# Performance work log

Hardware: AMD Instinct MI355X
Metric: run time of the kernel (lower is better)

The kernel has to match this reference:

```python
import jax, jax.numpy as jnp
import numpy as np

N, D, H, E = 16384, 2048, 1024, 16  # tokens, d_model, hidden_size, num_experts


def setup_inputs() -> dict:
    key = jax.random.key(0)
    k1, k2, k3 = jax.random.split(key, 3)
    x = jax.random.normal(k1, (N, D), dtype=jnp.float32)
    w_up_gate = jax.random.normal(k2, (E, 2 * H, D), dtype=jnp.float32) * 0.02
    w_down = jax.random.normal(k3, (E, H, D), dtype=jnp.float32) * 0.02
    # Tokens are pre-sorted by expert; uniform routing: N // E tokens per expert.
    batch_size_per_expert = jnp.full((E,), N // E, dtype=jnp.int32)
    return {
        "x": x,
        "w_up_gate": w_up_gate,
        "w_down": w_down,
        "batch_size_per_expert": batch_size_per_expert,
    }


def reference(x, w_up_gate, w_down, batch_size_per_expert):
    # Grouped GEMM expert FFN with SwiGLU (high-precision math path of
    # RoutedExperts.forward). Groups are uniform (N // E tokens each), so the
    # grouped matmul gmm(x, w.T, batch_sizes) is exactly a batched einsum over
    # the expert-contiguous token blocks.
    n_experts = w_up_gate.shape[0]
    hidden = w_down.shape[1]
    xg = x.reshape(n_experts, -1, x.shape[-1])            # [E, T, D]
    # up-gate projection: x_e @ w_up_gate[e].T -> [E, T, 2H]
    up_gate = jnp.einsum("etd,ehd->eth", xg, w_up_gate)
    up = up_gate[..., :hidden]                             # [E, T, H]
    gate = up_gate[..., hidden:]                           # [E, T, H]
    h = up * jax.nn.silu(gate)                             # fused SwiGLU
    # down projection: h_e @ w_down[e] -> [E, T, D]
    down = jnp.einsum("eth,ehd->etd", h, w_down)
    return down.reshape(x.shape)
```

## Files before the change

kernel.cpp:

```cpp
#include <hip/hip_runtime.h>
#include <hip/hip_bf16.h>

#define NE 16
#define NT 1024
#define ND 2048
#define NH 1024

typedef __bf16 bf16x8 __attribute__((ext_vector_type(8)));
typedef __bf16 bf16x4 __attribute__((ext_vector_type(4)));
typedef float  f32x4  __attribute__((ext_vector_type(4)));

__device__ __forceinline__ void async_load16(const __bf16* g, __bf16* l) {
  __builtin_amdgcn_global_load_lds(
      (const __attribute__((address_space(1))) void*)g,
      (__attribute__((address_space(3))) void*)l, 16, 0, 0);
}

template<bool CBF16>
__global__ __launch_bounds__(256, 2)
void gemm_nt_lds(const __bf16* __restrict__ Ap, const __bf16* __restrict__ Bp,
                 void* __restrict__ Cp, int K, long sA, long sB, long sC)
{
  __shared__ __bf16 As[128 * 32];
  __shared__ __bf16 Bs[128 * 32];

  const int tid  = threadIdx.x;
  const int lane = tid & 63;
  const int wave = tid >> 6;
  const int wr = wave >> 1, wc = wave & 1;
  const int m0 = blockIdx.y * 128;
  const int n0 = blockIdx.x * 128;
  const long zb = blockIdx.z;

  const __bf16* A = Ap + zb * sA + (long)m0 * K;
  const __bf16* B = Bp + zb * sB + (long)n0 * K;

  const int sr = lane >> 2;
  const int sc = (lane & 3) * 8;

  f32x4 acc[4][4] = {};
  const int kq  = (lane >> 4) * 8;
  const int l15 = lane & 15;

  for (int kk = 0; kk < K; kk += 32) {
    #pragma unroll
    for (int p = 0; p < 2; ++p) {
      const int slab = wave * 2 + p;
      const int r = slab * 16 + sr;
      async_load16(A + (long)r * K + kk + sc, &As[slab * 512]);
      async_load16(B + (long)r * K + kk + sc, &Bs[slab * 512]);
    }
    __syncthreads();

    bf16x8 af[4], bq[4];
    #pragma unroll
    for (int i = 0; i < 4; ++i)
      af[i] = *(const bf16x8*)(&As[(wr * 64 + i * 16 + l15) * 32 + kq]);
    #pragma unroll
    for (int j = 0; j < 4; ++j)
      bq[j] = *(const bf16x8*)(&Bs[(wc * 64 + j * 16 + l15) * 32 + kq]);
    #pragma unroll
    for (int i = 0; i < 4; ++i)
      #pragma unroll
      for (int j = 0; j < 4; ++j)
        acc[i][j] = __builtin_amdgcn_mfma_f32_16x16x32_bf16(af[i], bq[j], acc[i][j], 0, 0, 0);
    __syncthreads();
  }

  const int rq = (lane >> 4) * 4;
  if constexpr (CBF16) {
    __bf16* C = (__bf16*)Cp + zb * sC;
    #pragma unroll
    for (int i = 0; i < 4; ++i)
      #pragma unroll
      for (int j = 0; j < 4; ++j)
        #pragma unroll
        for (int r = 0; r < 4; ++r)
          C[(long)(m0 + wr * 64 + i * 16 + rq + r) * 2048 +
            (n0 + wc * 64 + j * 16 + l15)] = (__bf16)acc[i][j][r];
  } else {
    float* C = (float*)Cp + zb * sC;
    #pragma unroll
    for (int i = 0; i < 4; ++i)
      #pragma unroll
      for (int j = 0; j < 4; ++j)
        #pragma unroll
        for (int r = 0; r < 4; ++r)
          C[(long)(m0 + wr * 64 + i * 16 + rq + r) * 2048 +
            (n0 + wc * 64 + j * 16 + l15)] = acc[i][j][r];
  }
}

constexpr int LDSS = 40;
template<bool AF32, bool BF32, bool CBF16>
__global__ __launch_bounds__(256, 2)
void gemm_nt(const void* __restrict__ Ap, const void* __restrict__ Bp,
             void* __restrict__ Cp, int K, long sA, long sB, long sC)
{
  __shared__ __bf16 As[128 * LDSS];
  __shared__ __bf16 Bs[128 * LDSS];
  const int tid  = threadIdx.x;
  const int lane = tid & 63;
  const int wave = tid >> 6;
  const int wr = wave >> 1, wc = wave & 1;
  const int m0 = blockIdx.y * 128;
  const int n0 = blockIdx.x * 128;
  const long zb = blockIdx.z;
  f32x4 acc[4][4] = {};
  const int kq  = (lane >> 4) * 8;
  const int l15 = lane & 15;

  for (int kk = 0; kk < K; kk += 32) {
    if constexpr (AF32) {
      const float* A = (const float*)Ap + zb * sA + (long)m0 * K + kk;
      #pragma unroll
      for (int p = 0; p < 4; ++p) {
        const int r = p * 32 + (tid >> 3);
        const int c = (tid & 7) * 4;
        const float4 v = *(const float4*)(A + (long)r * K + c);
        bf16x4 w;
        w[0] = (__bf16)v.x; w[1] = (__bf16)v.y; w[2] = (__bf16)v.z; w[3] = (__bf16)v.w;
        *(bf16x4*)(&As[r * LDSS + c]) = w;
      }
    } else {
      const __bf16* A = (const __bf16*)Ap + zb * sA + (long)m0 * K + kk;
      #pragma unroll
      for (int p = 0; p < 2; ++p) {
        const int r = p * 64 + (tid >> 2);
        const int c = (tid & 3) * 8;
        *(bf16x8*)(&As[r * LDSS + c]) = *(const bf16x8*)(A + (long)r * K + c);
      }
    }
    if constexpr (BF32) {
      const float* B = (const float*)Bp + zb * sB + (long)n0 * K + kk;
      #pragma unroll
      for (int p = 0; p < 4; ++p) {
        const int r = p * 32 + (tid >> 3);
        const int c = (tid & 7) * 4;
        const float4 v = *(const float4*)(B + (long)r * K + c);
        bf16x4 w;
        w[0] = (__bf16)v.x; w[1] = (__bf16)v.y; w[2] = (__bf16)v.z; w[3] = (__bf16)v.w;
        *(bf16x4*)(&Bs[r * LDSS + c]) = w;
      }
    } else {
      const __bf16* B = (const __bf16*)Bp + zb * sB + (long)n0 * K + kk;
      #pragma unroll
      for (int p = 0; p < 2; ++p) {
        const int r = p * 64 + (tid >> 2);
        const int c = (tid & 3) * 8;
        *(bf16x8*)(&Bs[r * LDSS + c]) = *(const bf16x8*)(B + (long)r * K + c);
      }
    }
    __syncthreads();
    bf16x8 af[4], bq[4];
    #pragma unroll
    for (int i = 0; i < 4; ++i)
      af[i] = *(const bf16x8*)(&As[(wr * 64 + i * 16 + l15) * LDSS + kq]);
    #pragma unroll
    for (int j = 0; j < 4; ++j)
      bq[j] = *(const bf16x8*)(&Bs[(wc * 64 + j * 16 + l15) * LDSS + kq]);
    #pragma unroll
    for (int i = 0; i < 4; ++i)
      #pragma unroll
      for (int j = 0; j < 4; ++j)
        acc[i][j] = __builtin_amdgcn_mfma_f32_16x16x32_bf16(af[i], bq[j], acc[i][j], 0, 0, 0);
    __syncthreads();
  }
  const int rq = (lane >> 4) * 4;
  if constexpr (CBF16) {
    __bf16* C = (__bf16*)Cp + zb * sC;
    #pragma unroll
    for (int i = 0; i < 4; ++i)
      #pragma unroll
      for (int j = 0; j < 4; ++j)
        #pragma unroll
        for (int r = 0; r < 4; ++r)
          C[(long)(m0 + wr * 64 + i * 16 + rq + r) * 2048 +
            (n0 + wc * 64 + j * 16 + l15)] = (__bf16)acc[i][j][r];
  } else {
    float* C = (float*)Cp + zb * sC;
    #pragma unroll
    for (int i = 0; i < 4; ++i)
      #pragma unroll
      for (int j = 0; j < 4; ++j)
        #pragma unroll
        for (int r = 0; r < 4; ++r)
          C[(long)(m0 + wr * 64 + i * 16 + rq + r) * 2048 +
            (n0 + wc * 64 + j * 16 + l15)] = acc[i][j][r];
  }
}

__global__ __launch_bounds__(256)
void cast_f32_bf16(const float* __restrict__ src, __bf16* __restrict__ dst)
{
  const long i = ((long)blockIdx.x * 256 + threadIdx.x) * 8;
  const float4 a = *(const float4*)(src + i);
  const float4 b = *(const float4*)(src + i + 4);
  bf16x8 o;
  o[0] = (__bf16)a.x; o[1] = (__bf16)a.y; o[2] = (__bf16)a.z; o[3] = (__bf16)a.w;
  o[4] = (__bf16)b.x; o[5] = (__bf16)b.y; o[6] = (__bf16)b.z; o[7] = (__bf16)b.w;
  *(bf16x8*)(dst + i) = o;
}

__global__ __launch_bounds__(256)
void transpose_cast_wdown(const float* __restrict__ w, __bf16* __restrict__ wt)
{
  __shared__ __bf16 lt[64][72];
  const int e  = blockIdx.z;
  const int hb = blockIdx.y * 64;
  const int db = blockIdx.x * 64;
  const int tid = threadIdx.x;
  const int r  = tid >> 2;
  const int cq = (tid & 3) * 16;

  const float* src = w + (long)e * NH * ND + (long)(hb + r) * ND + db + cq;
  #pragma unroll
  for (int q = 0; q < 4; ++q) {
    const float4 v = *(const float4*)(src + q * 4);
    lt[cq + q * 4 + 0][r] = (__bf16)v.x;
    lt[cq + q * 4 + 1][r] = (__bf16)v.y;
    lt[cq + q * 4 + 2][r] = (__bf16)v.z;
    lt[cq + q * 4 + 3][r] = (__bf16)v.w;
  }
  __syncthreads();
  __bf16* dst = wt + (long)e * ND * NH + (long)(db + r) * NH + hb + cq;
  *(bf16x8*)(dst)     = *(const bf16x8*)(&lt[r][cq]);
  *(bf16x8*)(dst + 8) = *(const bf16x8*)(&lt[r][cq + 8]);
}

__global__ __launch_bounds__(256)
void silu_mul(const __bf16* __restrict__ ug, __bf16* __restrict__ h)
{
  const long g  = (long)blockIdx.x * 256 + threadIdx.x;
  const int  c8 = (int)(g & 127) * 8;
  const long row = g >> 7;
  const bf16x8 u  = *(const bf16x8*)(ug + row * 2048 + c8);
  const bf16x8 gt = *(const bf16x8*)(ug + row * 2048 + 1024 + c8);
  bf16x8 o;
  #pragma unroll
  for (int i = 0; i < 8; ++i) {
    const float uu = (float)u[i];
    const float gg = (float)gt[i];
    const float s  = gg / (1.0f + __expf(-gg));
    o[i] = (__bf16)(uu * s);
  }
  *(bf16x8*)(h + row * 1024 + c8) = o;
}

extern "C" void kernel_launch(void* const* d_in, const int* in_sizes, int n_in,
                              void* d_out, int out_size, void* d_ws, size_t ws_size,
                              hipStream_t stream) {
  const float* x   = (const float*)d_in[0];
  const float* wug = (const float*)d_in[1];
  const float* wdn = (const float*)d_in[2];
  float* out = (float*)d_out;

  const size_t MB = 1024 * 1024;
  char* ws = (char*)d_ws;
  __bf16* wdT = (__bf16*)(ws);
  __bf16* ug  = (__bf16*)(ws + 64 * MB);
  __bf16* hbf = (__bf16*)(ws + 128 * MB);

  transpose_cast_wdown<<<dim3(ND / 64, NH / 64, NE), 256, 0, stream>>>(wdn, wdT);

  if (ws_size >= 352 * MB) {
    __bf16* xbf   = (__bf16*)(ws + 160 * MB);
    __bf16* wugbf = (__bf16*)(ws + 224 * MB);

    cast_f32_bf16<<<16384, 256, 0, stream>>>(x, xbf);
    cast_f32_bf16<<<32768, 256, 0, stream>>>(wug, wugbf);

    gemm_nt_lds<true><<<dim3(2 * NH / 128, NT / 128, NE), 256, 0, stream>>>(
        xbf, wugbf, ug, ND, (long)NT * ND, (long)2 * NH * ND, (long)NT * 2 * NH);

    silu_mul<<<(NE * NT * NH / 8) / 256, 256, 0, stream>>>(ug, hbf);

    gemm_nt_lds<false><<<dim3(ND / 128, NT / 128, NE), 256, 0, stream>>>(
        hbf, wdT, out, NH, (long)NT * NH, (long)ND * NH, (long)NT * ND);
  } else {
    gemm_nt<true, true, true><<<dim3(2 * NH / 128, NT / 128, NE), 256, 0, stream>>>(
        x, wug, ug, ND, (long)NT * ND, (long)2 * NH * ND, (long)NT * 2 * NH);

    silu_mul<<<(NE * NT * NH / 8) / 256, 256, 0, stream>>>(ug, hbf);

    gemm_nt<false, false, false><<<dim3(ND / 128, NT / 128, NE), 256, 0, stream>>>(
        hbf, wdT, out, NH, (long)NT * NH, (long)ND * NH, (long)NT * ND);
  }
}
```

Before: 854.3 us.

## Use 256x256 tiles with 4-stage async LDS pipeline and swizzled layout

New measurement: 798.6 us. 1.07x faster.

```diff
diff --git a/kernel.cpp b/kernel.cpp
--- a/kernel.cpp
+++ b/kernel.cpp
@@ -17,76 +17,94 @@
 }
 
 template<bool CBF16>
-__global__ __launch_bounds__(256, 2)
-void gemm_nt_lds(const __bf16* __restrict__ Ap, const __bf16* __restrict__ Bp,
+__global__ __launch_bounds__(512, 2)
+void gemm_nt_256(const __bf16* __restrict__ Ap, const __bf16* __restrict__ Bp,
                  void* __restrict__ Cp, int K, long sA, long sB, long sC)
 {
-  __shared__ __bf16 As[128 * 32];
-  __shared__ __bf16 Bs[128 * 32];
+  __shared__ __bf16 sm[4 * 16384];
 
   const int tid  = threadIdx.x;
   const int lane = tid & 63;
   const int wave = tid >> 6;
-  const int wr = wave >> 1, wc = wave & 1;
-  const int m0 = blockIdx.y * 128;
-  const int n0 = blockIdx.x * 128;
+  const int wr = wave >> 2, wc = wave & 3;
+  const int m0 = blockIdx.y * 256;
+  const int n0 = blockIdx.x * 256;
   const long zb = blockIdx.z;
 
   const __bf16* A = Ap + zb * sA + (long)m0 * K;
   const __bf16* B = Bp + zb * sB + (long)n0 * K;
 
-  const int sr = lane >> 2;
-  const int sc = (lane & 3) * 8;
-
-  f32x4 acc[4][4] = {};
-  const int kq  = (lane >> 4) * 8;
+  const int srow = tid >> 2;
+  const int scol = ((tid & 3) ^ ((tid >> 3) & 3)) * 8;
+  const __bf16* As0 = A + (long)srow * K + scol;
+  const __bf16* Bs0 = B + (long)srow * K + scol;
+  const long h1 = (long)128 * K;
+  __bf16* ldst = &sm[wave * 512];
+
+  const int KT = K >> 5;
+
   const int l15 = lane & 15;
-
-  for (int kk = 0; kk < K; kk += 32) {
-    #pragma unroll
-    for (int p = 0; p < 2; ++p) {
-      const int slab = wave * 2 + p;
-      const int r = slab * 16 + sr;
-      async_load16(A + (long)r * K + kk + sc, &As[slab * 512]);
-      async_load16(B + (long)r * K + kk + sc, &Bs[slab * 512]);
-    }
-    __syncthreads();
-
-    bf16x8 af[4], bq[4];
-    #pragma unroll
-    for (int i = 0; i < 4; ++i)
-      af[i] = *(const bf16x8*)(&As[(wr * 64 + i * 16 + l15) * 32 + kq]);
+  const int rsl = ((lane >> 4) ^ ((l15 >> 1) & 3)) * 8;
+
+  f32x4 acc[8][4] = {};
+
+  auto stage = [&](int t) {
+    const int bb  = (t & 3) * 16384;
+    const long kk = (long)(t << 5);
+    async_load16(As0 + kk,      ldst + bb);
+    async_load16(As0 + kk + h1, ldst + bb + 4096);
+    async_load16(Bs0 + kk,      ldst + bb + 8192);
+    async_load16(Bs0 + kk + h1, ldst + bb + 12288);
+  };
+
+  stage(0); stage(1); stage(2);
+
+  for (int t = 0; t < KT; ++t) {
+    if (t < KT - 2)       asm volatile("s_waitcnt vmcnt(8)" ::: "memory");
+    else if (t == KT - 2) asm volatile("s_waitcnt vmcnt(4)" ::: "memory");
+    else                  asm volatile("s_waitcnt vmcnt(0)" ::: "memory");
+    __builtin_amdgcn_s_barrier();
+    __builtin_amdgcn_sched_barrier(0);
+    if (t + 3 < KT) stage(t + 3);
+
+    const int bb = (t & 3) * 16384;
+    bf16x8 af[8], bq[4];
+    #pragma unroll
+    for (int i = 0; i < 8; ++i)
+      af[i] = *(const bf16x8*)(&sm[bb + (wr * 128 + i * 16 + l15) * 32 + rsl]);
     #pragma unroll
     for (int j = 0; j < 4; ++j)
-      bq[j] = *(const bf16x8*)(&Bs[(wc * 64 + j * 16 + l15) * 32 + kq]);
-    #pragma unroll
-    for (int i = 0; i < 4; ++i)
+      bq[j] = *(const bf16x8*)(&sm[bb + 8192 + (wc * 64 + j * 16 + l15) * 32 + rsl]);
+
+    __builtin_amdgcn_s_setprio(1);
+    #pragma unroll
+    for (int i = 0; i < 8; ++i)
       #pragma unroll
       for (int j = 0; j < 4; ++j)
         acc[i][j] = __builtin_amdgcn_mfma_f32_16x16x32_bf16(af[i], bq[j], acc[i][j], 0, 0, 0);
-    __syncthreads();
+    __builtin_amdgcn_s_setprio(0);
   }
 
   const int rq = (lane >> 4) * 4;
   if constexpr (CBF16) {
     __bf16* C = (__bf16*)Cp + zb * sC;
     #pragma unroll
-    for (int i = 0; i < 4; ++i)
+    for (int i = 0; i < 8; ++i)
       #pragma unroll
       for (int j = 0; j < 4; ++j)
         #pragma unroll
         for (int r = 0; r < 4; ++r)
-          C[(long)(m0 + wr * 64 + i * 16 + rq + r) * 2048 +
+          C[(long)(m0 + wr * 128 + i * 16 + rq + r) * 2048 +
             (n0 + wc * 64 + j * 16 + l15)] = (__bf16)acc[i][j][r];
   } else {
     float* C = (float*)Cp + zb * sC;
     #pragma unroll
-    for (int i = 0; i < 4; ++i)
+    for (int i = 0; i < 8; ++i)
       #pragma unroll
       for (int j = 0; j < 4; ++j)
         #pragma unroll
         for (int r = 0; r < 4; ++r)
-          C[(long)(m0 + wr * 64 + i * 16 + rq + r) * 2048 +
+          C[(long)(m0 + wr * 128 + i * 16 + rq + r) * 2048 +
             (n0 + wc * 64 + j * 16 + l15)] = acc[i][j][r];
   }
 }
@@ -270,12 +288,12 @@
     cast_f32_bf16<<<16384, 256, 0, stream>>>(x, xbf);
     cast_f32_bf16<<<32768, 256, 0, stream>>>(wug, wugbf);
 
-    gemm_nt_lds<true><<<dim3(2 * NH / 128, NT / 128, NE), 256, 0, stream>>>(
+    gemm_nt_256<true><<<dim3(2 * NH / 256, NT / 256, NE), 512, 0, stream>>>(
         xbf, wugbf, ug, ND, (long)NT * ND, (long)2 * NH * ND, (long)NT * 2 * NH);
 
     silu_mul<<<(NE * NT * NH / 8) / 256, 256, 0, stream>>>(ug, hbf);
 
-    gemm_nt_lds<false><<<dim3(ND / 128, NT / 128, NE), 256, 0, stream>>>(
+    gemm_nt_256<false><<<dim3(ND / 256, NT / 256, NE), 512, 0, stream>>>(
         hbf, wdT, out, NH, (long)NT * NH, (long)ND * NH, (long)NT * ND);
   } else {
     gemm_nt<true, true, true><<<dim3(2 * NH / 128, NT / 128, NE), 256, 0, stream>>>(
```
